# Kernel tuning notes

Measured on AMD Instinct MI355X. Metric: run time of the kernel, lower is better.

The kernel has to match this reference:

```python
import jax, jax.numpy as jnp
import numpy as np

EPS = 1e-5

def setup_inputs() -> dict:
    key = jax.random.key(0)
    k1, k2 = jax.random.split(key)
    B, S, F = 16, 8192, 256
    x = jax.random.normal(k1, (B, S, F), dtype=jnp.float32)
    change_points = (jax.random.uniform(k2, (B, S)) < 0.001).astype(jnp.int32)
    affine_weight = jnp.ones((F,), dtype=jnp.float32)
    affine_bias = jnp.zeros((F,), dtype=jnp.float32)
    return {"x": x, "affine_weight": affine_weight, "affine_bias": affine_bias,
            "change_points": change_points}


def _segment_normalize(x, affine_weight, affine_bias, change_points):
    # x: [B, S, F]; change_points: [B, S] int
    B, S, F = x.shape
    # Torch loop: a boundary fires at position i (i >= 1) if ANY batch has a cp.
    ind = (jnp.sum(change_points, axis=0) > 0).astype(jnp.int32)  # [S]
    ind = ind.at[0].set(0)  # loop starts at i=1; position 0 never splits
    seg_id = jnp.cumsum(ind)  # [S], segment index shared across batch

    xt = jnp.swapaxes(x, 0, 1)  # [S, B, F]
    ones = jnp.ones((S,), dtype=x.dtype)
    counts = jax.ops.segment_sum(ones, seg_id, num_segments=S)  # [S]
    ssum = jax.ops.segment_sum(xt, seg_id, num_segments=S)      # [S, B, F]
    ssq = jax.ops.segment_sum(xt * xt, seg_id, num_segments=S)  # [S, B, F]
    cnt = jnp.maximum(counts, 1.0)[:, None, None]
    mean = ssum / cnt                                   # per-segment mean (biased var)
    var = jnp.maximum(ssq / cnt - mean * mean, 0.0)
    std = jnp.sqrt(var + EPS)
    # stats are .detach()ed in the original
    mean_t = jax.lax.stop_gradient(mean)[seg_id]  # gather back to [S, B, F]
    std_t = jax.lax.stop_gradient(std)[seg_id]
    xn = (xt - mean_t) / std_t
    xn = jnp.swapaxes(xn, 0, 1)  # [B, S, F]
    xn = xn * affine_weight + affine_bias
    return xn


def reference(x, affine_weight, affine_bias, change_points):
    return _segment_normalize(x, affine_weight, affine_bias, change_points)
```

## Files before the change

kernel.cpp:

```cpp
#include <hip/hip_runtime.h>

#define BSZ 16
#define SSZ 8192
#define F4  64
#define EPSV 1e-5f
#define SEGCAP 256
#define CHCAP  384
#define CH 64
#define NBLK_S 4096
#define NBLK_N 2048

typedef float f32x4 __attribute__((ext_vector_type(4)));

__global__ void cp_reduce_kernel(const int* __restrict__ cp, int* __restrict__ ind) {
    int s = blockIdx.x * blockDim.x + threadIdx.x;
    if (s >= SSZ) return;
    int a = 0;
#pragma unroll
    for (int b = 0; b < BSZ; ++b) a |= cp[b * SSZ + s];
    ind[s] = (s == 0) ? 0 : (a != 0 ? 1 : 0);
}

__global__ __launch_bounds__(1024) void scan_kernel(const int* __restrict__ ind,
                                                    int* __restrict__ ch_s0,
                                                    int* __restrict__ ch_s1,
                                                    int* __restrict__ ch_c0,
                                                    int* __restrict__ ch_n,
                                                    int* __restrict__ ch_seg,
                                                    float* __restrict__ ch_rc,
                                                    int* __restrict__ seg_id,
                                                    int* __restrict__ ctr,
                                                    int* __restrict__ meta) {
    __shared__ int ldsi[1024];
    __shared__ int sstart[SEGCAP];
    __shared__ int snseg;
    const int t = threadIdx.x;
    for (int i = t; i < CHCAP * BSZ; i += 1024) ctr[i] = 0;

    int vals[8];
    int tot = 0;
#pragma unroll
    for (int i = 0; i < 8; ++i) { int v = ind[t * 8 + i]; vals[i] = v; tot += v; }
    ldsi[t] = tot;
    __syncthreads();
    for (int off = 1; off < 1024; off <<= 1) {
        int a = ldsi[t];
        int b = (t >= off) ? ldsi[t - off] : 0;
        __syncthreads();
        ldsi[t] = a + b;
        __syncthreads();
    }
    int run = ldsi[t] - tot;
#pragma unroll
    for (int i = 0; i < 8; ++i) {
        run += vals[i];
        int r = run < SEGCAP ? run : SEGCAP - 1;
        if (vals[i] && run < SEGCAP) sstart[run] = t * 8 + i;
        seg_id[t * 8 + i] = r;
    }
    if (t == 0) sstart[0] = 0;
    if (t == 1023) { int n = ldsi[1023] + 1; snseg = n < SEGCAP ? n : SEGCAP; }
    __syncthreads();

    const int nseg = snseg;
    int st = 0, en = 0, nch = 0;
    if (t < nseg) {
        st = sstart[t];
        en = (t + 1 < nseg) ? sstart[t + 1] : SSZ;
        nch = (en - st + CH - 1) / CH;
    }
    ldsi[t] = nch;
    __syncthreads();
    for (int off = 1; off < 1024; off <<= 1) {
        int a = ldsi[t];
        int b = (t >= off) ? ldsi[t - off] : 0;
        __syncthreads();
        ldsi[t] = a + b;
        __syncthreads();
    }
    const int cbase = ldsi[t] - nch;
    if (t < nseg) {
        const float rc = 1.0f / (float)(en - st);
        for (int j = 0; j < nch; ++j) {
            const int c = cbase + j;
            ch_s0[c] = st + j * CH;
            ch_s1[c] = min(en, st + (j + 1) * CH);
            ch_c0[c] = cbase;
            ch_n[c]  = nch;
            ch_seg[c] = t;
            ch_rc[c] = rc;
        }
    }
    if (t == 1023) meta[0] = ldsi[1023] * BSZ;
}

__global__ __launch_bounds__(256) void stats_kernel(const f32x4* __restrict__ x4,
                                                    const int* __restrict__ ch_s0,
                                                    const int* __restrict__ ch_s1,
                                                    const int* __restrict__ ch_c0,
                                                    const int* __restrict__ ch_n,
                                                    const int* __restrict__ ch_seg,
                                                    const float* __restrict__ ch_rc,
                                                    const int* __restrict__ meta,
                                                    float* __restrict__ psum,
                                                    float* __restrict__ pssq,
                                                    int* __restrict__ ctr,
                                                    f32x4* __restrict__ mean4,
                                                    f32x4* __restrict__ rstd4) {
    __shared__ f32x4 lsum[4][64];
    __shared__ f32x4 lssq[4][64];
    __shared__ int lcloser;
    const int nitems = meta[0];
    const int lane = threadIdx.x & 63;
    const int wave = threadIdx.x >> 6;
    for (int item = blockIdx.x; item < nitems; item += NBLK_S) {
        const int c = item >> 4;
        const int b = item & 15;
        const int s0 = ch_s0[c], s1 = ch_s1[c];
        const int n = ch_n[c];
        const int seg = ch_seg[c];
        const float rc = ch_rc[c];
        const f32x4* px = x4 + (size_t)b * SSZ * F4 + lane;

        f32x4 sum = {0.f, 0.f, 0.f, 0.f};
        f32x4 ssq = {0.f, 0.f, 0.f, 0.f};
        for (int s = s0 + wave; s < s1; s += 4) {
            f32x4 v = px[(size_t)s * F4];
            sum += v;
            ssq += v * v;
        }
        lsum[wave][lane] = sum;
        lssq[wave][lane] = ssq;
        __syncthreads();

        if (n == 1) {
            if (wave == 0) {
                f32x4 S = lsum[0][lane] + lsum[1][lane] + lsum[2][lane] + lsum[3][lane];
                f32x4 Q = lssq[0][lane] + lssq[1][lane] + lssq[2][lane] + lssq[3][lane];
                f32x4 m = S * rc;
                f32x4 var = Q * rc - m * m;
                f32x4 r;
                r.x = 1.0f / sqrtf(fmaxf(var.x, 0.f) + EPSV);
                r.y = 1.0f / sqrtf(fmaxf(var.y, 0.f) + EPSV);
                r.z = 1.0f / sqrtf(fmaxf(var.z, 0.f) + EPSV);
                r.w = 1.0f / sqrtf(fmaxf(var.w, 0.f) + EPSV);
                mean4[((size_t)seg * BSZ + b) * F4 + lane] = m;
                rstd4[((size_t)seg * BSZ + b) * F4 + lane] = r;
            }
            __syncthreads();
        } else {
            const int c0 = ch_c0[c];
            const size_t pb = ((size_t)c * BSZ + b) * F4 * 4 + lane * 4;
            if (wave == 0) {
                f32x4 o = lsum[0][lane] + lsum[1][lane] + lsum[2][lane] + lsum[3][lane];
#pragma unroll
                for (int j = 0; j < 4; ++j)
                    __hip_atomic_store(&psum[pb + j], o[j], __ATOMIC_RELAXED,
                                       __HIP_MEMORY_SCOPE_AGENT);
            } else if (wave == 1) {
                f32x4 o = lssq[0][lane] + lssq[1][lane] + lssq[2][lane] + lssq[3][lane];
#pragma unroll
                for (int j = 0; j < 4; ++j)
                    __hip_atomic_store(&pssq[pb + j], o[j], __ATOMIC_RELAXED,
                                       __HIP_MEMORY_SCOPE_AGENT);
            }
            __syncthreads();
            if (threadIdx.x == 0) {
                int ret = __hip_atomic_fetch_add(&ctr[c0 * BSZ + b], 1,
                                                 __ATOMIC_RELAXED,
                                                 __HIP_MEMORY_SCOPE_AGENT);
                lcloser = (ret == n - 1);
            }
            __syncthreads();
            if (lcloser && wave == 0) {
                f32x4 S = {0.f, 0.f, 0.f, 0.f};
                f32x4 Q = {0.f, 0.f, 0.f, 0.f};
                for (int cc = c0; cc < c0 + n; ++cc) {
                    const size_t qb = ((size_t)cc * BSZ + b) * F4 * 4 + lane * 4;
#pragma unroll
                    for (int j = 0; j < 4; ++j) {
                        S[j] += __hip_atomic_load(&psum[qb + j], __ATOMIC_RELAXED,
                                                  __HIP_MEMORY_SCOPE_AGENT);
                        Q[j] += __hip_atomic_load(&pssq[qb + j], __ATOMIC_RELAXED,
                                                  __HIP_MEMORY_SCOPE_AGENT);
                    }
                }
                f32x4 m = S * rc;
                f32x4 var = Q * rc - m * m;
                f32x4 r;
                r.x = 1.0f / sqrtf(fmaxf(var.x, 0.f) + EPSV);
                r.y = 1.0f / sqrtf(fmaxf(var.y, 0.f) + EPSV);
                r.z = 1.0f / sqrtf(fmaxf(var.z, 0.f) + EPSV);
                r.w = 1.0f / sqrtf(fmaxf(var.w, 0.f) + EPSV);
                mean4[((size_t)seg * BSZ + b) * F4 + lane] = m;
                rstd4[((size_t)seg * BSZ + b) * F4 + lane] = r;
            }
            __syncthreads();
        }
    }
}

__global__ __launch_bounds__(256) void norm_kernel(const f32x4* __restrict__ x4,
                                                   const f32x4* __restrict__ w4p,
                                                   const f32x4* __restrict__ b4p,
                                                   const int* __restrict__ seg_id,
                                                   const f32x4* __restrict__ mean4,
                                                   const f32x4* __restrict__ rstd4,
                                                   f32x4* __restrict__ out4) {
    int tid = blockIdx.x * blockDim.x + threadIdx.x;
    int f4i = tid & 63;
    int s = tid >> 6;
    f32x4 w = w4p[f4i];
    f32x4 bb = b4p[f4i];
    int seg = seg_id[s];
    size_t xi = (size_t)s * F4 + f4i;
    int mi = (seg * BSZ) * F4 + f4i;
#pragma unroll
    for (int b = 0; b < BSZ; ++b) {
        f32x4 v = x4[xi + (size_t)b * SSZ * F4];
        f32x4 m = mean4[mi + b * F4];
        f32x4 r = rstd4[mi + b * F4];
        f32x4 o = (v - m) * r * w + bb;
        __builtin_nontemporal_store(o, &out4[xi + (size_t)b * SSZ * F4]);
    }
}

extern "C" void kernel_launch(void* const* d_in, const int* in_sizes, int n_in,
                              void* d_out, int out_size, void* d_ws, size_t ws_size,
                              hipStream_t stream) {
    const f32x4* x = (const f32x4*)d_in[0];
    const f32x4* w = (const f32x4*)d_in[1];
    const f32x4* bias = (const f32x4*)d_in[2];
    const int* cp = (const int*)d_in[3];

    char* ws = (char*)d_ws;
    int*   meta  = (int*)ws;
    int*   ch_s0 = (int*)(ws + 2048);
    int*   ch_s1 = (int*)(ws + 4096);
    int*   ch_c0 = (int*)(ws + 6144);
    int*   ch_n  = (int*)(ws + 8192);
    int*   ch_seg= (int*)(ws + 10240);
    float* ch_rc = (float*)(ws + 12288);
    int*   ctr   = (int*)(ws + 32768);
    int*   seg_id= (int*)(ws + 65536);
    int*   ind   = (int*)(ws + 98304);
    float* psum  = (float*)(ws + 131072);
    float* pssq  = psum + (size_t)CHCAP * BSZ * F4 * 4;
    f32x4* mean4 = (f32x4*)(pssq + (size_t)CHCAP * BSZ * F4 * 4);
    f32x4* rstd4 = mean4 + (size_t)SEGCAP * BSZ * F4;

    cp_reduce_kernel<<<32, 256, 0, stream>>>(cp, ind);
    scan_kernel<<<1, 1024, 0, stream>>>(ind, ch_s0, ch_s1, ch_c0, ch_n, ch_seg,
                                        ch_rc, seg_id, ctr, meta);
    stats_kernel<<<NBLK_S, 256, 0, stream>>>(x, ch_s0, ch_s1, ch_c0, ch_n, ch_seg,
                                             ch_rc, meta, psum, pssq, ctr,
                                             mean4, rstd4);
    norm_kernel<<<NBLK_N, 256, 0, stream>>>(x, w, bias, seg_id, mean4, rstd4,
                                            (f32x4*)d_out);
}
```

Baseline: 93.48 us.

## Fuse change-point reduction into scan, use wave-shuffle scans, flatten norm grid

Folds the change-point OR-reduction into the single-block scan kernel, which reads cp with int4 loads. The LDS Hillis-Steele scans are replaced by wave shuffle scans plus a 16-entry cross-wave combine, which cuts the number of barriers. The norm kernel now uses one thread per output float4 across all batches with a much larger grid, instead of each thread looping over 16 batches. This removes one launch and the scan latency, at the cost of a single block reading 512KB of cp and more redundant weight, bias and seg_id loads per thread in norm.

```diff
diff --git a/kernel.cpp b/kernel.cpp
--- a/kernel.cpp
+++ b/kernel.cpp
@@ -8,20 +8,33 @@
 #define CHCAP  384
 #define CH 64
 #define NBLK_S 4096
-#define NBLK_N 2048
 
 typedef float f32x4 __attribute__((ext_vector_type(4)));
 
-__global__ void cp_reduce_kernel(const int* __restrict__ cp, int* __restrict__ ind) {
-    int s = blockIdx.x * blockDim.x + threadIdx.x;
-    if (s >= SSZ) return;
-    int a = 0;
-#pragma unroll
-    for (int b = 0; b < BSZ; ++b) a |= cp[b * SSZ + s];
-    ind[s] = (s == 0) ? 0 : (a != 0 ? 1 : 0);
-}
-
-__global__ __launch_bounds__(1024) void scan_kernel(const int* __restrict__ ind,
+__device__ __forceinline__ int wave_scan_incl(int x) {
+    const int lane = threadIdx.x & 63;
+#pragma unroll
+    for (int o = 1; o < 64; o <<= 1) {
+        int v = __shfl_up(x, o, 64);
+        if (lane >= o) x += v;
+    }
+    return x;
+}
+
+__device__ __forceinline__ int block_scan_incl(int x, int* lds16) {
+    const int wid = threadIdx.x >> 6;
+    const int lane = threadIdx.x & 63;
+    int w = wave_scan_incl(x);
+    if (lane == 63) lds16[wid] = w;
+    __syncthreads();
+    int base = 0;
+#pragma unroll
+    for (int j = 0; j < 16; ++j) base += (j < wid) ? lds16[j] : 0;
+    __syncthreads();
+    return base + w;
+}
+
+__global__ __launch_bounds__(1024) void scan_kernel(const int* __restrict__ cp,
                                                     int* __restrict__ ch_s0,
                                                     int* __restrict__ ch_s1,
                                                     int* __restrict__ ch_c0,
@@ -31,26 +44,34 @@
                                                     int* __restrict__ seg_id,
                                                     int* __restrict__ ctr,
                                                     int* __restrict__ meta) {
-    __shared__ int ldsi[1024];
+    __shared__ int lds16[16];
     __shared__ int sstart[SEGCAP];
     __shared__ int snseg;
+    __shared__ int stot;
     const int t = threadIdx.x;
     for (int i = t; i < CHCAP * BSZ; i += 1024) ctr[i] = 0;
 
     int vals[8];
+    {
+        const int4* cp4 = (const int4*)cp;
+        int4 a0 = {0, 0, 0, 0}, a1 = {0, 0, 0, 0};
+#pragma unroll
+        for (int b = 0; b < BSZ; ++b) {
+            int4 u = cp4[b * 2048 + t * 2];
+            int4 v = cp4[b * 2048 + t * 2 + 1];
+            a0.x |= u.x; a0.y |= u.y; a0.z |= u.z; a0.w |= u.w;
+            a1.x |= v.x; a1.y |= v.y; a1.z |= v.z; a1.w |= v.w;
+        }
+        vals[0] = a0.x != 0; vals[1] = a0.y != 0; vals[2] = a0.z != 0; vals[3] = a0.w != 0;
+        vals[4] = a1.x != 0; vals[5] = a1.y != 0; vals[6] = a1.z != 0; vals[7] = a1.w != 0;
+        if (t == 0) vals[0] = 0;
+    }
     int tot = 0;
 #pragma unroll
-    for (int i = 0; i < 8; ++i) { int v = ind[t * 8 + i]; vals[i] = v; tot += v; }
-    ldsi[t] = tot;
-    __syncthreads();
-    for (int off = 1; off < 1024; off <<= 1) {
-        int a = ldsi[t];
-        int b = (t >= off) ? ldsi[t - off] : 0;
-        __syncthreads();
-        ldsi[t] = a + b;
-        __syncthreads();
-    }
-    int run = ldsi[t] - tot;
+    for (int i = 0; i < 8; ++i) tot += vals[i];
+
+    const int incl = block_scan_incl(tot, lds16);
+    int run = incl - tot;
 #pragma unroll
     for (int i = 0; i < 8; ++i) {
         run += vals[i];
@@ -59,7 +80,7 @@
         seg_id[t * 8 + i] = r;
     }
     if (t == 0) sstart[0] = 0;
-    if (t == 1023) { int n = ldsi[1023] + 1; snseg = n < SEGCAP ? n : SEGCAP; }
+    if (t == 1023) { int n = incl + 1; snseg = n < SEGCAP ? n : SEGCAP; }
     __syncthreads();
 
     const int nseg = snseg;
@@ -69,16 +90,8 @@
         en = (t + 1 < nseg) ? sstart[t + 1] : SSZ;
         nch = (en - st + CH - 1) / CH;
     }
-    ldsi[t] = nch;
-    __syncthreads();
-    for (int off = 1; off < 1024; off <<= 1) {
-        int a = ldsi[t];
-        int b = (t >= off) ? ldsi[t - off] : 0;
-        __syncthreads();
-        ldsi[t] = a + b;
-        __syncthreads();
-    }
-    const int cbase = ldsi[t] - nch;
+    const int incl2 = block_scan_incl(nch, lds16);
+    const int cbase = incl2 - nch;
     if (t < nseg) {
         const float rc = 1.0f / (float)(en - st);
         for (int j = 0; j < nch; ++j) {
@@ -91,7 +104,9 @@
             ch_rc[c] = rc;
         }
     }
-    if (t == 1023) meta[0] = ldsi[1023] * BSZ;
+    if (t == 1023) stot = incl2;
+    __syncthreads();
+    if (t == 0) meta[0] = stot * BSZ;
 }
 
 __global__ __launch_bounds__(256) void stats_kernel(const f32x4* __restrict__ x4,
@@ -207,22 +222,18 @@
                                                    const f32x4* __restrict__ mean4,
                                                    const f32x4* __restrict__ rstd4,
                                                    f32x4* __restrict__ out4) {
-    int tid = blockIdx.x * blockDim.x + threadIdx.x;
-    int f4i = tid & 63;
-    int s = tid >> 6;
-    f32x4 w = w4p[f4i];
-    f32x4 bb = b4p[f4i];
-    int seg = seg_id[s];
-    size_t xi = (size_t)s * F4 + f4i;
-    int mi = (seg * BSZ) * F4 + f4i;
-#pragma unroll
-    for (int b = 0; b < BSZ; ++b) {
-        f32x4 v = x4[xi + (size_t)b * SSZ * F4];
-        f32x4 m = mean4[mi + b * F4];
-        f32x4 r = rstd4[mi + b * F4];
-        f32x4 o = (v - m) * r * w + bb;
-        __builtin_nontemporal_store(o, &out4[xi + (size_t)b * SSZ * F4]);
-    }
+    const int tid = blockIdx.x * 256 + threadIdx.x;
+    const int f4i = tid & 63;
+    const int s = (tid >> 6) & (SSZ - 1);
+    const int b = tid >> 19;
+    const int seg = seg_id[s];
+    const f32x4 m = mean4[((size_t)seg * BSZ + b) * F4 + f4i];
+    const f32x4 r = rstd4[((size_t)seg * BSZ + b) * F4 + f4i];
+    const f32x4 w = w4p[f4i];
+    const f32x4 bb = b4p[f4i];
+    const f32x4 v = x4[(size_t)tid];
+    f32x4 o = (v - m) * r * w + bb;
+    __builtin_nontemporal_store(o, &out4[(size_t)tid]);
 }
 
 extern "C" void kernel_launch(void* const* d_in, const int* in_sizes, int n_in,
@@ -243,18 +254,17 @@
     float* ch_rc = (float*)(ws + 12288);
     int*   ctr   = (int*)(ws + 32768);
     int*   seg_id= (int*)(ws + 65536);
-    int*   ind   = (int*)(ws + 98304);
     float* psum  = (float*)(ws + 131072);
     float* pssq  = psum + (size_t)CHCAP * BSZ * F4 * 4;
     f32x4* mean4 = (f32x4*)(pssq + (size_t)CHCAP * BSZ * F4 * 4);
     f32x4* rstd4 = mean4 + (size_t)SEGCAP * BSZ * F4;
 
-    cp_reduce_kernel<<<32, 256, 0, stream>>>(cp, ind);
-    scan_kernel<<<1, 1024, 0, stream>>>(ind, ch_s0, ch_s1, ch_c0, ch_n, ch_seg,
+    scan_kernel<<<1, 1024, 0, stream>>>(cp, ch_s0, ch_s1, ch_c0, ch_n, ch_seg,
                                         ch_rc, seg_id, ctr, meta);
     stats_kernel<<<NBLK_S, 256, 0, stream>>>(x, ch_s0, ch_s1, ch_c0, ch_n, ch_seg,
                                              ch_rc, meta, psum, pssq, ctr,
                                              mean4, rstd4);
-    norm_kernel<<<NBLK_N, 256, 0, stream>>>(x, w, bias, seg_id, mean4, rstd4,
-                                            (f32x4*)d_out);
-}
+    norm_kernel<<<BSZ * SSZ * F4 / 256, 256, 0, stream>>>(x, w, bias, seg_id,
+                                                          mean4, rstd4,
+                                                          (f32x4*)d_out);
+}
```

Result: no change. 92.23 us (median of 2 runs) (-1.3%).
